# Kernel tuning notes

Measured on AMD Instinct MI355X. Metric: run time of the kernel, lower is better.

The kernel has to match this reference:

```python
import jax, jax.numpy as jnp
import numpy as np

N_HEAD = 16
LN_EPS = 1e-5


def _layernorm(x, g, b):
    mu = jnp.mean(x, axis=-1, keepdims=True)
    var = jnp.mean(jnp.square(x - mu), axis=-1, keepdims=True)
    return (x - mu) * jax.lax.rsqrt(var + LN_EPS) * g + b


def setup_inputs() -> dict:
    key = jax.random.key(0)
    ks = jax.random.split(key, 8)
    B, T, C = 2, 2048, 1024
    Dff = 4 * C
    s = 0.02
    return {
        "x": jax.random.normal(ks[0], (B, T, C), jnp.float32),
        "wq": jax.random.normal(ks[1], (C, C), jnp.float32) * s,
        "wk": jax.random.normal(ks[2], (C, C), jnp.float32) * s,
        "wv": jax.random.normal(ks[3], (C, C), jnp.float32) * s,
        "w_proj": jax.random.normal(ks[4], (C, C), jnp.float32) * s,
        "b_proj": jnp.zeros((C,), jnp.float32),
        "w1": jax.random.normal(ks[5], (C, Dff), jnp.float32) * s,
        "b1": jnp.zeros((Dff,), jnp.float32),
        "w2": jax.random.normal(ks[6], (Dff, C), jnp.float32) * s,
        "b2": jnp.zeros((C,), jnp.float32),
        "g1": jnp.ones((C,), jnp.float32),
        "be1": jnp.zeros((C,), jnp.float32),
        "g2": jnp.ones((C,), jnp.float32),
        "be2": jnp.zeros((C,), jnp.float32),
    }


def reference(x, wq, wk, wv, w_proj, b_proj, w1, b1, w2, b2, g1, be1, g2, be2):
    B, T, C = x.shape
    H = N_HEAD
    hd = C // H
    # QKV projections (all heads folded into one matmul each), -> [B,H,T,hd]
    q = (x @ wq).reshape(B, T, H, hd).transpose(0, 2, 1, 3)
    k = (x @ wk).reshape(B, T, H, hd).transpose(0, 2, 1, 3)
    v = (x @ wv).reshape(B, T, H, hd).transpose(0, 2, 1, 3)
    # scaled causal attention; scale = head_size ** -0.5 as in torch source
    scores = jnp.einsum("bhqd,bhkd->bhqk", q, k) * (hd ** -0.5)
    causal = jnp.tril(jnp.ones((T, T), bool))
    scores = jnp.where(causal, scores, jnp.finfo(scores.dtype).min)
    wei = jax.nn.softmax(scores, axis=-1)
    attn = jnp.einsum("bhqk,bhkd->bhqd", wei, v)  # [B,H,T,hd]
    attn = attn.transpose(0, 2, 1, 3).reshape(B, T, C)
    y = attn @ w_proj + b_proj
    # post-LN residuals as in Block.forward
    x = _layernorm(x + y, g1, be1)
    y = jnp.maximum(x @ w1 + b1, 0.0) @ w2 + b2
    x = _layernorm(x + y, g2, be2)
    return x
```

## Files before the change

kernel.cpp:

```cpp
#include <hip/hip_runtime.h>
#include <hip/hip_bf16.h>


typedef __attribute__((ext_vector_type(8))) short bf16x8;
typedef __attribute__((ext_vector_type(4))) float f32x4;
typedef __attribute__((ext_vector_type(4))) short short4v;

__device__ inline short f2bf(float f) {
    __hip_bfloat16 h = __float2bfloat16(f);
    return *reinterpret_cast<short*>(&h);
}
__device__ inline float bf2f(short s) {
    union { unsigned u; float f; } c;
    c.u = ((unsigned)(unsigned short)s) << 16;
    return c.f;
}

__global__ __launch_bounds__(256) void mega_prep(const float* __restrict__ x,
                                                 short* __restrict__ x_bf,
                                                 const float* __restrict__ wq,
                                                 const float* __restrict__ wk,
                                                 const float* __restrict__ wv,
                                                 const float* __restrict__ wp,
                                                 short* __restrict__ wqT,
                                                 short* __restrict__ wkT,
                                                 short* __restrict__ wvT,
                                                 short* __restrict__ wpT,
                                                 const float* __restrict__ w1,
                                                 short* __restrict__ w1T,
                                                 const float* __restrict__ w2,
                                                 short* __restrict__ w2T,
                                                 float scaleq) {
    const int blk = blockIdx.x;
    const int tid = threadIdx.x;
    if (blk < 4096) {
        const int i = blk * 256 + tid;
        float4 v = *(const float4*)(x + (size_t)i * 4);
        short4v o = { f2bf(v.x), f2bf(v.y), f2bf(v.z), f2bf(v.w) };
        *(short4v*)(x_bf + (size_t)i * 4) = o;
        return;
    }
    __shared__ short tile[32][33];
    const int tx = tid & 31, ty = tid >> 5;
    const float* in;
    short* out;
    int R, C, bx, by;
    float scale = 1.0f;
    if (blk < 8192) {
        const int b2 = blk - 4096;
        const int z = b2 >> 10;
        const int rem = b2 & 1023;
        bx = rem & 31; by = rem >> 5;
        R = 1024; C = 1024;
        in = z == 0 ? wq : z == 1 ? wk : z == 2 ? wv : wp;
        out = z == 0 ? wqT : z == 1 ? wkT : z == 2 ? wvT : wpT;
        if (z == 0) scale = scaleq;
    } else if (blk < 12288) {
        const int rem = blk - 8192;
        bx = rem & 127; by = rem >> 7;
        R = 1024; C = 4096;
        in = w1; out = w1T;
    } else {
        const int rem = blk - 12288;
        bx = rem & 31; by = rem >> 5;
        R = 4096; C = 1024;
        in = w2; out = w2T;
    }
    const int c0 = bx * 32, r0 = by * 32;
    for (int i = ty; i < 32; i += 8)
        tile[i][tx] = f2bf(in[(size_t)(r0 + i) * C + c0 + tx] * scale);
    __syncthreads();
    for (int i = ty; i < 32; i += 8)
        out[(size_t)(c0 + i) * R + r0 + tx] = tile[tx][i];
}

template <int BN, int BIAS, int RELU, int OUTBF>
__device__ __forceinline__ void gemm_core(const short* __restrict__ A,
                                          const short* __restrict__ BT,
                                          const float* __restrict__ bias,
                                          void* __restrict__ Cout,
                                          int N, int K, int lda, int ldb,
                                          int gx, int w,
                                          short* As, short* Bs, bool addbias) {
    constexpr int NI = BN / 32;
    const int tid = threadIdx.x;
    const int wid = tid >> 6;
    const int lane = tid & 63;
    const int wr = wid >> 1, wc = wid & 1;
    const int row0 = (w % gx) * 128;
    const int col0 = (w / gx) * BN;
    const int lr = lane & 15;
    const int lk = (lane >> 4) * 8;
    const int sr = lane >> 3;
    const int scs = ((lane & 7) * 8) ^ (sr * 8);
    const int rsw = (lr & 7) * 8;

    f32x4 acc[4][NI] = {};
    for (int k = 0; k < K; k += 64) {
#pragma unroll
        for (int c = 0; c < 4; ++c) {
            const int ch = wid + c * 4;
            const short* ga = A + (size_t)(row0 + ch * 8 + sr) * lda + k + scs;
            __builtin_amdgcn_global_load_lds(
                (const __attribute__((address_space(1))) unsigned int*)ga,
                (__attribute__((address_space(3))) unsigned int*)(As + ch * 512), 16, 0, 0);
        }
#pragma unroll
        for (int c = 0; c < BN / 32; ++c) {
            const int ch = wid + c * 4;
            const short* gb = BT + (size_t)(col0 + ch * 8 + sr) * ldb + k + scs;
            __builtin_amdgcn_global_load_lds(
                (const __attribute__((address_space(1))) unsigned int*)gb,
                (__attribute__((address_space(3))) unsigned int*)(Bs + ch * 512), 16, 0, 0);
        }
        __syncthreads();
#pragma unroll
        for (int kk = 0; kk < 64; kk += 32) {
            const int cof = (kk + lk) ^ rsw;
            bf16x8 a[4], b[NI];
#pragma unroll
            for (int m = 0; m < 4; ++m)
                a[m] = *(const bf16x8*)(As + (wr * 64 + m * 16 + lr) * 64 + cof);
#pragma unroll
            for (int n = 0; n < NI; ++n)
                b[n] = *(const bf16x8*)(Bs + (wc * (BN / 2) + n * 16 + lr) * 64 + cof);
#pragma unroll
            for (int m = 0; m < 4; ++m)
#pragma unroll
                for (int n = 0; n < NI; ++n)
                    acc[m][n] = __builtin_amdgcn_mfma_f32_16x16x32_bf16(a[m], b[n], acc[m][n], 0, 0, 0);
        }
        __syncthreads();
    }
#pragma unroll
    for (int m = 0; m < 4; ++m) {
        int row = row0 + wr * 64 + m * 16 + (lane >> 4) * 4;
#pragma unroll
        for (int n = 0; n < NI; ++n) {
            int col = col0 + wc * (BN / 2) + n * 16 + lr;
            float bv = (BIAS && addbias) ? bias[col] : 0.0f;
#pragma unroll
            for (int r = 0; r < 4; ++r) {
                float v = acc[m][n][r] + bv;
                if (RELU) v = fmaxf(v, 0.0f);
                if (OUTBF)
                    ((short*)Cout)[(size_t)(row + r) * N + col] = f2bf(v);
                else
                    ((float*)Cout)[(size_t)(row + r) * N + col] = v;
            }
        }
    }
}

template <int BN, int BIAS, int RELU, int OUTBF>
__global__ __launch_bounds__(256) void gemm_bt(const short* __restrict__ A,
                                               const short* __restrict__ BT,
                                               const float* __restrict__ bias,
                                               void* __restrict__ Cout,
                                               int N, int K, int lda, int ldb,
                                               void* __restrict__ Cout2) {
    __shared__ short As[128 * 64];
    __shared__ short Bs[BN * 64];
    const int kz = blockIdx.z;
    if (kz) { A += K; BT += K; Cout = Cout2; }
    const int gx = gridDim.x;
    int flat = blockIdx.x + gx * blockIdx.y;
    const int nwg = gx * gridDim.y;
    int w = flat;
    if ((nwg & 7) == 0) {
        const int q = nwg >> 3;
        w = (flat & 7) * q + (flat >> 3);
    }
    gemm_core<BN, BIAS, RELU, OUTBF>(A, BT, bias, Cout, N, K, lda, ldb, gx, w, As, Bs, kz == 0);
}

__global__ __launch_bounds__(256) void gemm_qkv_vt(const short* __restrict__ x_bf,
                                                   const short* __restrict__ wqkT,
                                                   const short* __restrict__ wvT,
                                                   short* __restrict__ qk,
                                                   short* __restrict__ Vt) {
    __shared__ short As[128 * 64];
    __shared__ short Bs[128 * 64];
    int flat = blockIdx.x;
    if (flat < 512) {
        const int w = (flat & 7) * 64 + (flat >> 3);
        gemm_core<128, 0, 0, 1>(x_bf, wqkT, nullptr, qk, 2048, 1024, 1024, 1024, 32, w, As, Bs, false);
    } else {
        flat -= 512;
        const int w = (flat & 7) * 32 + (flat >> 3);
        gemm_core<128, 0, 0, 1>(wvT, x_bf, nullptr, Vt, 4096, 1024, 1024, 1024, 8, w, As, Bs, false);
    }
}

#define ATT_T 2048
#define ATT_QKS 2048
#define ATT_BT 4096

#define LOADK(KF, KB)                                                                     \
    do {                                                                                  \
        const int k0_ = (KB) * 64;                                                        \
        _Pragma("unroll") for (int t = 0; t < 4; ++t) {                                   \
            const size_t krow_ = (size_t)(b * ATT_T + k0_ + 16 * t + lr) * ATT_QKS + h * 64; \
            KF[t][0] = *(const bf16x8*)(Km + krow_ + g * 8);                              \
            KF[t][1] = *(const bf16x8*)(Km + krow_ + 32 + g * 8);                         \
        }                                                                                 \
    } while (0)

#define LOADV(VF, KB)                                                                     \
    do {                                                                                  \
        const int k0_ = (KB) * 64;                                                        \
        _Pragma("unroll") for (int n = 0; n < 4; ++n)                                     \
            _Pragma("unroll") for (int ks = 0; ks < 2; ++ks)                              \
                VF[n][ks] = *(const bf16x8*)(Vt + (size_t)(h * 64 + n * 16 + lr) * ATT_BT + \
                                             b * ATT_T + k0_ + ks * 32 + g * 8);          \
    } while (0)

#define COMPUTE(KF, VF, KB)                                                               \
    do {                                                                                  \
        const int k0_ = (KB) * 64;                                                        \
        const bool edge_ = (KB) == nfull;                                                 \
        _Pragma("unroll") for (int qs = 0; qs < 2; ++qs) {                                \
            f32x4 st[4];                                                                  \
            __builtin_amdgcn_s_setprio(1);                                                \
            _Pragma("unroll") for (int t = 0; t < 4; ++t) {                               \
                f32x4 s = {};                                                             \
                s = __builtin_amdgcn_mfma_f32_16x16x32_bf16(KF[t][0], aq[qs][0], s, 0, 0, 0); \
                s = __builtin_amdgcn_mfma_f32_16x16x32_bf16(KF[t][1], aq[qs][1], s, 0, 0, 0); \
                st[t] = s;                                                                \
            }                                                                             \
            __builtin_amdgcn_s_setprio(0);                                                \
            float rs = 0.0f;                                                              \
            _Pragma("unroll") for (int t = 0; t < 4; ++t) {                               \
                short4v pw;                                                               \
                _Pragma("unroll") for (int r = 0; r < 4; ++r) {                           \
                    float val = st[t][r];                                                 \
                    if (edge_ && (k0_ + 16 * t + g * 4 + r > qrow[qs])) val = -3e38f;     \
                    float p = exp2f(val);                                                 \
                    rs += p;                                                              \
                    pw[r] = f2bf(p);                                                      \
                }                                                                         \
                *(short4v*)(&Plds[wid][qs][lr][16 * t + g * 4]) = pw;                     \
            }                                                                             \
            rs += __shfl_xor(rs, 16);                                                     \
            rs += __shfl_xor(rs, 32);                                                     \
            lrun[qs] += rs;                                                               \
        }                                                                                 \
        asm volatile("s_waitcnt lgkmcnt(0)" ::: "memory");                                \
        __builtin_amdgcn_sched_barrier(0);                                                \
        __builtin_amdgcn_s_setprio(1);                                                    \
        _Pragma("unroll") for (int qs = 0; qs < 2; ++qs)                                  \
            _Pragma("unroll") for (int ks = 0; ks < 2; ++ks) {                            \
                bf16x8 pf = *(const bf16x8*)(&Plds[wid][qs][lr][ks * 32 + g * 8]);        \
                _Pragma("unroll") for (int n = 0; n < 4; ++n)                             \
                    O[qs][n] = __builtin_amdgcn_mfma_f32_16x16x32_bf16(VF[n][ks], pf, O[qs][n], 0, 0, 0); \
            }                                                                             \
        __builtin_amdgcn_s_setprio(0);                                                    \
    } while (0)

__global__ __launch_bounds__(128) void flash_attn(const short* __restrict__ Q,
                                                  const short* __restrict__ Km,
                                                  const short* __restrict__ Vt,
                                                  short* __restrict__ Oout) {
    const int f = blockIdx.x;
    const int wid = threadIdx.x >> 6;
    const int lane = threadIdx.x & 63;
    const int lr = lane & 15;
    const int g = lane >> 4;
    const int xcd = f & 7;
    const int k = f >> 3;
    const int bh = xcd * 4 + (k & 3);
    const int b = bh >> 4;
    const int h = bh & 15;
    const int pair = (k >> 2) * 2 + wid;

    __shared__ __align__(16) short Plds[2][2][16][72];

#pragma unroll 1
    for (int job = 0; job < 2; ++job) {
        const int s = job ? (63 - pair) : pair;
        const int q0 = s << 5;
        const int qrow[2] = { q0 + lr, q0 + 16 + lr };
        const int nfull = s >> 1;

        bf16x8 aq[2][2];
#pragma unroll
        for (int qs = 0; qs < 2; ++qs)
#pragma unroll
            for (int ds = 0; ds < 2; ++ds)
                aq[qs][ds] = *(const bf16x8*)(Q + (size_t)(b * ATT_T + q0 + qs * 16 + lr) * ATT_QKS +
                                              h * 64 + ds * 32 + g * 8);

        f32x4 O[2][4] = {};
        float lrun[2] = { 0.0f, 0.0f };

        bf16x8 kfA[4][2], kfB[4][2], vf[4][2];
        LOADK(kfA, 0);
        int kb = 0;
        while (true) {
            LOADV(vf, kb);
            if (kb < nfull) LOADK(kfB, kb + 1);
            COMPUTE(kfA, vf, kb);
            ++kb;
            if (kb > nfull) break;
            LOADV(vf, kb);
            if (kb < nfull) LOADK(kfA, kb + 1);
            COMPUTE(kfB, vf, kb);
            ++kb;
            if (kb > nfull) break;
        }

#pragma unroll
        for (int qs = 0; qs < 2; ++qs) {
            const float inv = 1.0f / lrun[qs];
#pragma unroll
            for (int n = 0; n < 4; ++n) {
                short4v ov;
#pragma unroll
                for (int r = 0; r < 4; ++r) ov[r] = f2bf(O[qs][n][r] * inv);
                *(short4v*)(Oout + (size_t)(b * ATT_T + q0 + qs * 16 + lr) * 1024 +
                            h * 64 + n * 16 + g * 4) = ov;
            }
        }
    }
}

__global__ __launch_bounds__(256) void resid_ln(const float* __restrict__ x,
                                                const short* __restrict__ y,
                                                const short* __restrict__ yb,
                                                const float* __restrict__ g,
                                                const float* __restrict__ be,
                                                float* __restrict__ of,
                                                short* __restrict__ ob) {
    const int row = blockIdx.x;
    const int tid = threadIdx.x;
    const size_t base = (size_t)row * 1024 + tid * 4;
    float4 xv = *(const float4*)(x + base);
    short4v yv = *(const short4v*)(y + base);
    float h0 = xv.x + bf2f(yv[0]), h1 = xv.y + bf2f(yv[1]);
    float h2 = xv.z + bf2f(yv[2]), h3 = xv.w + bf2f(yv[3]);
    if (yb) {
        short4v bv2 = *(const short4v*)(yb + base);
        h0 += bf2f(bv2[0]); h1 += bf2f(bv2[1]); h2 += bf2f(bv2[2]); h3 += bf2f(bv2[3]);
    }
    float s = h0 + h1 + h2 + h3;
    float ss = h0 * h0 + h1 * h1 + h2 * h2 + h3 * h3;
#pragma unroll
    for (int d = 1; d < 64; d <<= 1) {
        s += __shfl_xor(s, d);
        ss += __shfl_xor(ss, d);
    }
    __shared__ float as_[4], ass_[4];
    if ((tid & 63) == 0) { as_[tid >> 6] = s; ass_[tid >> 6] = ss; }
    __syncthreads();
    s = as_[0] + as_[1] + as_[2] + as_[3];
    ss = ass_[0] + ass_[1] + ass_[2] + ass_[3];
    const float mu = s * (1.0f / 1024.0f);
    const float var = ss * (1.0f / 1024.0f) - mu * mu;
    const float rstd = rsqrtf(var + 1e-5f);
    float4 gv = *(const float4*)(g + tid * 4);
    float4 bv = *(const float4*)(be + tid * 4);
    float o0 = (h0 - mu) * rstd * gv.x + bv.x;
    float o1 = (h1 - mu) * rstd * gv.y + bv.y;
    float o2 = (h2 - mu) * rstd * gv.z + bv.z;
    float o3 = (h3 - mu) * rstd * gv.w + bv.w;
    float4 ov = { o0, o1, o2, o3 };
    *(float4*)(of + base) = ov;
    if (ob) {
        short4v obv = { f2bf(o0), f2bf(o1), f2bf(o2), f2bf(o3) };
        *(short4v*)(ob + base) = obv;
    }
}


extern "C" void kernel_launch(void* const* d_in, const int* in_sizes, int n_in,
                              void* d_out, int out_size, void* d_ws, size_t ws_size,
                              hipStream_t stream) {
    const float* x = (const float*)d_in[0];
    const float* wq = (const float*)d_in[1];
    const float* wk = (const float*)d_in[2];
    const float* wv = (const float*)d_in[3];
    const float* wp = (const float*)d_in[4];
    const float* bproj = (const float*)d_in[5];
    const float* w1 = (const float*)d_in[6];
    const float* b1 = (const float*)d_in[7];
    const float* w2 = (const float*)d_in[8];
    const float* b2 = (const float*)d_in[9];
    const float* g1 = (const float*)d_in[10];
    const float* be1 = (const float*)d_in[11];
    const float* g2 = (const float*)d_in[12];
    const float* be2 = (const float*)d_in[13];

    char* ws = (char*)d_ws;
    const size_t MB = 1024 * 1024;
    short* x_bf = (short*)(ws + 0);
    short* wqkT = (short*)(ws + 8 * MB);
    short* wqT = wqkT;
    short* wkT = (short*)(ws + 10 * MB);
    short* wvT = (short*)(ws + 12 * MB);
    short* w1T = (short*)(ws + 16 * MB);
    short* w2T = (short*)(ws + 24 * MB);
    short* qk  = (short*)(ws + 32 * MB);
    short* wpT = (short*)(ws + 48 * MB);
    short* Vt  = (short*)(ws + 56 * MB);
    short* hbf = (short*)(ws + 32 * MB);
    short* attn = (short*)(ws + 64 * MB);
    short* x1bf = (short*)(ws + 64 * MB);
    short* y1a = (short*)(ws + 72 * MB);
    short* y1b = (short*)(ws + 0);
    short* y2a = (short*)(ws + 72 * MB);
    short* y2b = (short*)(ws + 0);
    float* x1f = (float*)(ws + 88 * MB);

    dim3 blk(256);
    const float SC = 0.125f * 1.44269504089f;

    mega_prep<<<dim3(16384), blk, 0, stream>>>(x, x_bf, wq, wk, wv, wp,
                                               wqT, wkT, wvT, wpT,
                                               w1, w1T, w2, w2T, SC);
    gemm_qkv_vt<<<dim3(768), blk, 0, stream>>>(x_bf, wqkT, wvT, qk, Vt);
    flash_attn<<<dim3(512), dim3(128), 0, stream>>>(qk, qk + 1024, Vt, attn);
    gemm_bt<64, 1, 0, 1><<<dim3(32, 16, 2), blk, 0, stream>>>(attn, wpT, bproj, y1a,
                                                              1024, 512, 1024, 1024, y1b);
    resid_ln<<<dim3(4096), blk, 0, stream>>>(x, y1a, y1b, g1, be1, x1f, x1bf);
    gemm_bt<128, 1, 1, 1><<<dim3(32, 32), blk, 0, stream>>>(x1bf, w1T, b1, hbf,
                                                            4096, 1024, 1024, 1024, nullptr);
    gemm_bt<64, 1, 0, 1><<<dim3(32, 16, 2), blk, 0, stream>>>(hbf, w2T, b2, y2a,
                                                              1024, 2048, 4096, 4096, y2b);
    resid_ln<<<dim3(4096), blk, 0, stream>>>(x1f, y2a, y2b, g2, be2, (float*)d_out, nullptr);
}
```

Baseline: 283.8 us.

## Drop fp32 LN1 output, reuse bf16 residual, retile FFN1 GEMM, tree-sum row sums

The first residual+LayerNorm now writes only the bf16 copy, and the second LayerNorm reads that bf16 tensor as its residual, removing an fp32 write and read of the intermediate activation. The FFN up-projection GEMM tile is changed from 128 to 64 with double the grid in one dimension. The softmax row-sum in the attention kernel uses a tree of partial sums to shorten the dependency chain. The residual path now carries bf16 rounding error into the final output, which reduces accuracy.

```diff
diff --git a/kernel.cpp b/kernel.cpp
--- a/kernel.cpp
+++ b/kernel.cpp
@@ -229,18 +229,21 @@
                 st[t] = s;                                                                \
             }                                                                             \
             __builtin_amdgcn_s_setprio(0);                                                \
-            float rs = 0.0f;                                                              \
+            float rst[4];                                                                 \
             _Pragma("unroll") for (int t = 0; t < 4; ++t) {                               \
                 short4v pw;                                                               \
+                float pr[4];                                                              \
                 _Pragma("unroll") for (int r = 0; r < 4; ++r) {                           \
                     float val = st[t][r];                                                 \
                     if (edge_ && (k0_ + 16 * t + g * 4 + r > qrow[qs])) val = -3e38f;     \
                     float p = exp2f(val);                                                 \
-                    rs += p;                                                              \
+                    pr[r] = p;                                                            \
                     pw[r] = f2bf(p);                                                      \
                 }                                                                         \
+                rst[t] = (pr[0] + pr[1]) + (pr[2] + pr[3]);                               \
                 *(short4v*)(&Plds[wid][qs][lr][16 * t + g * 4]) = pw;                     \
             }                                                                             \
+            float rs = (rst[0] + rst[1]) + (rst[2] + rst[3]);                             \
             rs += __shfl_xor(rs, 16);                                                     \
             rs += __shfl_xor(rs, 32);                                                     \
             lrun[qs] += rs;                                                               \
@@ -324,7 +327,9 @@
     }
 }
 
-__global__ __launch_bounds__(256) void resid_ln(const float* __restrict__ x,
+template <int XB>
+__global__ __launch_bounds__(256) void resid_ln(const float* __restrict__ xf,
+                                                const short* __restrict__ xb,
                                                 const short* __restrict__ y,
                                                 const short* __restrict__ yb,
                                                 const float* __restrict__ g,
@@ -334,10 +339,17 @@
     const int row = blockIdx.x;
     const int tid = threadIdx.x;
     const size_t base = (size_t)row * 1024 + tid * 4;
-    float4 xv = *(const float4*)(x + base);
+    float x0, x1, x2, x3;
+    if (XB) {
+        short4v xv = *(const short4v*)(xb + base);
+        x0 = bf2f(xv[0]); x1 = bf2f(xv[1]); x2 = bf2f(xv[2]); x3 = bf2f(xv[3]);
+    } else {
+        float4 xv = *(const float4*)(xf + base);
+        x0 = xv.x; x1 = xv.y; x2 = xv.z; x3 = xv.w;
+    }
     short4v yv = *(const short4v*)(y + base);
-    float h0 = xv.x + bf2f(yv[0]), h1 = xv.y + bf2f(yv[1]);
-    float h2 = xv.z + bf2f(yv[2]), h3 = xv.w + bf2f(yv[3]);
+    float h0 = x0 + bf2f(yv[0]), h1 = x1 + bf2f(yv[1]);
+    float h2 = x2 + bf2f(yv[2]), h3 = x3 + bf2f(yv[3]);
     if (yb) {
         short4v bv2 = *(const short4v*)(yb + base);
         h0 += bf2f(bv2[0]); h1 += bf2f(bv2[1]); h2 += bf2f(bv2[2]); h3 += bf2f(bv2[3]);
@@ -363,8 +375,10 @@
     float o1 = (h1 - mu) * rstd * gv.y + bv.y;
     float o2 = (h2 - mu) * rstd * gv.z + bv.z;
     float o3 = (h3 - mu) * rstd * gv.w + bv.w;
-    float4 ov = { o0, o1, o2, o3 };
-    *(float4*)(of + base) = ov;
+    if (of) {
+        float4 ov = { o0, o1, o2, o3 };
+        *(float4*)(of + base) = ov;
+    }
     if (ob) {
         short4v obv = { f2bf(o0), f2bf(o1), f2bf(o2), f2bf(o3) };
         *(short4v*)(ob + base) = obv;
@@ -409,7 +423,6 @@
     short* y1b = (short*)(ws + 0);
     short* y2a = (short*)(ws + 72 * MB);
     short* y2b = (short*)(ws + 0);
-    float* x1f = (float*)(ws + 88 * MB);
 
     dim3 blk(256);
     const float SC = 0.125f * 1.44269504089f;
@@ -421,10 +434,12 @@
     flash_attn<<<dim3(512), dim3(128), 0, stream>>>(qk, qk + 1024, Vt, attn);
     gemm_bt<64, 1, 0, 1><<<dim3(32, 16, 2), blk, 0, stream>>>(attn, wpT, bproj, y1a,
                                                               1024, 512, 1024, 1024, y1b);
-    resid_ln<<<dim3(4096), blk, 0, stream>>>(x, y1a, y1b, g1, be1, x1f, x1bf);
-    gemm_bt<128, 1, 1, 1><<<dim3(32, 32), blk, 0, stream>>>(x1bf, w1T, b1, hbf,
-                                                            4096, 1024, 1024, 1024, nullptr);
+    resid_ln<0><<<dim3(4096), blk, 0, stream>>>(x, nullptr, y1a, y1b, g1, be1,
+                                                nullptr, x1bf);
+    gemm_bt<64, 1, 1, 1><<<dim3(32, 64), blk, 0, stream>>>(x1bf, w1T, b1, hbf,
+                                                           4096, 1024, 1024, 1024, nullptr);
     gemm_bt<64, 1, 0, 1><<<dim3(32, 16, 2), blk, 0, stream>>>(hbf, w2T, b2, y2a,
                                                               1024, 2048, 4096, 4096, y2b);
-    resid_ln<<<dim3(4096), blk, 0, stream>>>(x1f, y2a, y2b, g2, be2, (float*)d_out, nullptr);
-}
+    resid_ln<1><<<dim3(4096), blk, 0, stream>>>(nullptr, x1bf, y2a, y2b, g2, be2,
+                                                (float*)d_out, nullptr);
+}
```

After: 273.5 us. -3.6%, faster.
